# Kernel optimization log

Hardware: AMD Instinct MI355X
Metric: run time of the kernel (lower is better)

## Reference

```python
import jax, jax.numpy as jnp
import numpy as np

HIDDEN = 800
BETA = 0.95
SLOPE = 25.0

@jax.custom_vjp
def surrogate_spike(mem, thr):
    # hard threshold forward, sigmoid-derivative surrogate backward
    return (mem > thr).astype(mem.dtype)

def _spk_fwd(mem, thr):
    return surrogate_spike(mem, thr), (mem, thr)

def _spk_bwd(res, g):
    mem, thr = res
    s = jax.nn.sigmoid(SLOPE * (mem - thr))
    return (g * SLOPE * s * (1.0 - s), jnp.zeros_like(thr))

surrogate_spike.defvjp(_spk_fwd, _spk_bwd)


def setup_inputs() -> dict:
    key = jax.random.key(0)
    ks = jax.random.split(key, 6)
    T, B = 50, 512
    x = jax.random.normal(ks[0], (T, B, 784), dtype=jnp.float32)
    # Kaiming-ish init scaled by 1/sqrt(fan_in)
    W1 = jax.random.normal(ks[1], (HIDDEN, 784), dtype=jnp.float32) / np.sqrt(784.0)
    W2 = jax.random.normal(ks[2], (HIDDEN, HIDDEN), dtype=jnp.float32) / np.sqrt(float(HIDDEN))
    W3 = jax.random.normal(ks[3], (10, HIDDEN), dtype=jnp.float32) / np.sqrt(float(HIDDEN))
    b1 = jnp.zeros((HIDDEN,), jnp.float32)
    b2 = jnp.zeros((HIDDEN,), jnp.float32)
    b3 = jnp.zeros((10,), jnp.float32)
    budget1 = jax.random.uniform(ks[4], (HIDDEN,), dtype=jnp.float32)
    budget2 = jax.random.uniform(ks[5], (HIDDEN,), dtype=jnp.float32)
    return {"x": x, "W1": W1, "b1": b1, "W2": W2, "b2": b2,
            "W3": W3, "b3": b3, "budget1": budget1, "budget2": budget2}


def reference(x, W1, b1, W2, b2, W3, b3, budget1, budget2):
    # thresholds: 1 / clamp(budget / max_budget, 0.01, 1.0); max_budget = 1.0 here
    thr1 = 1.0 / jnp.clip(budget1, 0.01, 1.0)
    thr2 = 1.0 / jnp.clip(budget2, 0.01, 1.0)
    thr3 = jnp.asarray(1.0, x.dtype)
    B = x.shape[1]

    def step(carry, xt):
        m1, m2, m3 = carry
        m1 = BETA * m1 + xt @ W1.T + b1            # [B, HIDDEN]
        s1 = surrogate_spike(m1, thr1)
        m1 = m1 * (1.0 - s1)                        # multiplicative reset
        m2 = BETA * m2 + s1 @ W2.T + b2
        s2 = surrogate_spike(m2, thr2)
        m2 = m2 * (1.0 - s2)
        m3 = BETA * m3 + s2 @ W3.T + b3            # [B, 10]
        s3 = surrogate_spike(m3, thr3)
        m3 = m3 * (1.0 - s3)
        return (m1, m2, m3), (s1, s2, s3)

    init = (jnp.zeros((B, HIDDEN), x.dtype),
            jnp.zeros((B, HIDDEN), x.dtype),
            jnp.zeros((B, 10), x.dtype))
    _, (s1r, s2r, s3r) = jax.lax.scan(step, init, x)
    return (s3r.sum(0), s1r, s2r, s3r)
```

## Files before the change

kernel.cpp:

```cpp
#include <hip/hip_runtime.h>

#define BATCH   512
#define TSTEPS  50
#define NIN     784
#define NHID    800
#define NOUT    10
#define KC      384

typedef float v4f __attribute__((ext_vector_type(4)));

#define ROW_FMA(pl, ph, as)                       \
    pl.x = __fmaf_rn(as, blo.x, pl.x);            \
    pl.y = __fmaf_rn(as, blo.y, pl.y);            \
    pl.z = __fmaf_rn(as, blo.z, pl.z);            \
    pl.w = __fmaf_rn(as, blo.w, pl.w);            \
    ph.x = __fmaf_rn(as, bhi.x, ph.x);            \
    ph.y = __fmaf_rn(as, bhi.y, ph.y);            \
    ph.z = __fmaf_rn(as, bhi.z, ph.z);            \
    ph.w = __fmaf_rn(as, bhi.w, ph.w);

#define STORE_ROW(i, pl, ph)                                        \
    {   float* crow = Cp + (size_t)(m0 + 8*ty + (i)) * N + cb;      \
        if (cb + 4 <= N) *(float4*)crow = pl;                       \
        if (cb + 8 <= N) *(float4*)(crow + 4) = ph; }

__global__ __launch_bounds__(256, 2)
void gemm_panel_f32(const float* __restrict__ A, const float* __restrict__ B,
                    float* __restrict__ Cp, int M, int N, int K,
                    int ks, int ke)
{
    __shared__ float As[8][132];
    __shared__ float Bs[8][188];

    const int tid = threadIdx.x;
    const int tx = tid & 15;
    const int ty = tid >> 4;
    const int m0 = blockIdx.x * 128;
    const int n0 = blockIdx.y * 128;

    const int srow = tid >> 1;
    const int skq  = (tid & 1) * 4;
    const int bphys = 12 * (srow >> 3) + (srow & 7);

    const float* Aptr = A + (size_t)(m0 + srow) * K + skq;
    const float* Bptr = B + (size_t)(n0 + srow) * K + skq;
    const bool bval = (n0 + srow) < N;

    float4 p0l = {0,0,0,0}, p0h = {0,0,0,0}, p1l = {0,0,0,0}, p1h = {0,0,0,0};
    float4 p2l = {0,0,0,0}, p2h = {0,0,0,0}, p3l = {0,0,0,0}, p3h = {0,0,0,0};
    float4 p4l = {0,0,0,0}, p4h = {0,0,0,0}, p5l = {0,0,0,0}, p5h = {0,0,0,0};
    float4 p6l = {0,0,0,0}, p6h = {0,0,0,0}, p7l = {0,0,0,0}, p7h = {0,0,0,0};

    float4 av = *(const float4*)(Aptr + ks);
    float4 bv = bval ? *(const float4*)(Bptr + ks) : make_float4(0.f,0.f,0.f,0.f);

    for (int k0 = ks; k0 < ke; k0 += 8) {
        __syncthreads();
        As[skq+0][srow] = av.x; As[skq+1][srow] = av.y;
        As[skq+2][srow] = av.z; As[skq+3][srow] = av.w;
        Bs[skq+0][bphys] = bv.x; Bs[skq+1][bphys] = bv.y;
        Bs[skq+2][bphys] = bv.z; Bs[skq+3][bphys] = bv.w;
        __syncthreads();

        if (k0 + 8 < ke) {
            av = *(const float4*)(Aptr + k0 + 8);
            bv = bval ? *(const float4*)(Bptr + k0 + 8)
                      : make_float4(0.f,0.f,0.f,0.f);
        }

        #pragma unroll
        for (int kk = 0; kk < 8; ++kk) {
            const float4 alo = *(const float4*)&As[kk][8*ty];
            const float4 ahi = *(const float4*)&As[kk][8*ty + 4];
            const float4 blo = *(const float4*)&Bs[kk][12*tx];
            const float4 bhi = *(const float4*)&Bs[kk][12*tx + 4];
            ROW_FMA(p0l, p0h, alo.x)
            ROW_FMA(p1l, p1h, alo.y)
            ROW_FMA(p2l, p2h, alo.z)
            ROW_FMA(p3l, p3h, alo.w)
            ROW_FMA(p4l, p4h, ahi.x)
            ROW_FMA(p5l, p5h, ahi.y)
            ROW_FMA(p6l, p6h, ahi.z)
            ROW_FMA(p7l, p7h, ahi.w)
        }
    }

    const int cb = n0 + 8 * tx;
    STORE_ROW(0, p0l, p0h)
    STORE_ROW(1, p1l, p1h)
    STORE_ROW(2, p2l, p2h)
    STORE_ROW(3, p3l, p3h)
    STORE_ROW(4, p4l, p4h)
    STORE_ROW(5, p5l, p5h)
    STORE_ROW(6, p6l, p6h)
    STORE_ROW(7, p7l, p7h)
}

__global__ __launch_bounds__(256)
void transpose800(const float* __restrict__ W2, float* __restrict__ W2T)
{
    __shared__ float t[32][33];
    const int tx  = threadIdx.x & 31;
    const int ty8 = threadIdx.x >> 5;
    const int bx = blockIdx.x * 32, by = blockIdx.y * 32;

    #pragma unroll
    for (int r = 0; r < 4; ++r) {
        int a = ty8 + r * 8;
        t[a][tx] = W2[(size_t)(by + a) * 800 + bx + tx];
    }
    __syncthreads();
    #pragma unroll
    for (int r = 0; r < 4; ++r) {
        int a = ty8 + r * 8;
        W2T[(size_t)(bx + a) * 800 + by + tx] = t[tx][a];
    }
}

__global__ __launch_bounds__(256)
void lif_scan_hid1(const float* __restrict__ Z0,
                   const float* __restrict__ Z1,
                   const float* __restrict__ xc,
                   const float* __restrict__ W1,
                   const float* __restrict__ bias,
                   const float* __restrict__ budget,
                   float* __restrict__ mcarry,
                   float* __restrict__ Sout,
                   unsigned long long* __restrict__ bm,
                   int CT, int t0)
{
    __shared__ float W1s[NHID][17];

    const int b = blockIdx.x;
    const int tid = threadIdx.x;
    const int lane = tid & 63;
    const int wave = tid >> 6;

    for (int q = tid; q < NHID * 16; q += 256)
        W1s[q >> 4][q & 15] = W1[(size_t)(q >> 4) * NIN + 768 + (q & 15)];
    __syncthreads();

    float m[4], thr[4], bj[4];
    bool val[4];
    int jjv[4];
    #pragma unroll
    for (int c = 0; c < 4; ++c) {
        const int j = c * 256 + tid;
        val[c] = (j < NHID);
        const int jj = val[c] ? j : 0;
        jjv[c] = jj;
        float bu = budget[jj];
        bu = fminf(fmaxf(bu, 0.01f), 1.0f);
        thr[c] = __fdiv_rn(1.0f, bu);
        bj[c]  = bias[jj];
        m[c]   = mcarry[b * NHID + jj];
    }

    for (int ct = 0; ct < CT; ++ct) {
        const size_t zbase = (size_t)ct * (BATCH * NHID) + (size_t)b * NHID;
        const size_t sbase = (size_t)(t0 + ct) * (BATCH * NHID) + (size_t)b * NHID;
        const float* xr = xc + ((size_t)ct * BATCH + b) * NIN + 768;
        const float4 x0 = *(const float4*)(xr);
        const float4 x1 = *(const float4*)(xr + 4);
        const float4 x2 = *(const float4*)(xr + 8);
        const float4 x3 = *(const float4*)(xr + 12);

        #pragma unroll
        for (int c = 0; c < 4; ++c) {
            const int j = c * 256 + tid;
            bool sp = false;
            if (val[c]) {
                const int jj = jjv[c];
                float z = __fadd_rn(__builtin_nontemporal_load(Z0 + zbase + j),
                                    __builtin_nontemporal_load(Z1 + zbase + j));
                float p3 = 0.0f;
                p3 = __fmaf_rn(x0.x, W1s[jj][0],  p3);
                p3 = __fmaf_rn(x0.y, W1s[jj][1],  p3);
                p3 = __fmaf_rn(x0.z, W1s[jj][2],  p3);
                p3 = __fmaf_rn(x0.w, W1s[jj][3],  p3);
                p3 = __fmaf_rn(x1.x, W1s[jj][4],  p3);
                p3 = __fmaf_rn(x1.y, W1s[jj][5],  p3);
                p3 = __fmaf_rn(x1.z, W1s[jj][6],  p3);
                p3 = __fmaf_rn(x1.w, W1s[jj][7],  p3);
                p3 = __fmaf_rn(x2.x, W1s[jj][8],  p3);
                p3 = __fmaf_rn(x2.y, W1s[jj][9],  p3);
                p3 = __fmaf_rn(x2.z, W1s[jj][10], p3);
                p3 = __fmaf_rn(x2.w, W1s[jj][11], p3);
                p3 = __fmaf_rn(x3.x, W1s[jj][12], p3);
                p3 = __fmaf_rn(x3.y, W1s[jj][13], p3);
                p3 = __fmaf_rn(x3.z, W1s[jj][14], p3);
                p3 = __fmaf_rn(x3.w, W1s[jj][15], p3);
                z = __fadd_rn(z, p3);

                float mm = __fadd_rn(__fadd_rn(__fmul_rn(0.95f, m[c]), z), bj[c]);
                sp = (mm > thr[c]);
                m[c] = sp ? 0.0f : mm;
                __builtin_nontemporal_store(sp ? 1.0f : 0.0f, Sout + sbase + j);
            }
            unsigned long long bits = __ballot(sp);
            if (lane == 0) {
                const int W = c * 4 + wave;
                if (W < 13)
                    bm[((size_t)ct * BATCH + b) * 13 + W] = bits;
            }
        }
    }
    #pragma unroll
    for (int c = 0; c < 4; ++c)
        if (val[c]) mcarry[b * NHID + c * 256 + tid] = m[c];
}

__global__ __launch_bounds__(256)
void lif_scan_hid2(const float* __restrict__ Z0,
                   const float* __restrict__ bias,
                   const float* __restrict__ budget,
                   float* __restrict__ mcarry,
                   float* __restrict__ Sout,
                   int CT, int t0)
{
    const int b = blockIdx.x;
    const int tid = threadIdx.x;

    float m[4], thr[4], bj[4];
    bool val[4];
    #pragma unroll
    for (int c = 0; c < 4; ++c) {
        const int j = c * 256 + tid;
        val[c] = (j < NHID);
        const int jj = val[c] ? j : 0;
        float bu = budget[jj];
        bu = fminf(fmaxf(bu, 0.01f), 1.0f);
        thr[c] = __fdiv_rn(1.0f, bu);
        bj[c]  = bias[jj];
        m[c]   = mcarry[b * NHID + jj];
    }

    for (int ct = 0; ct < CT; ++ct) {
        const size_t zbase = (size_t)ct * (BATCH * NHID) + (size_t)b * NHID;
        const size_t sbase = (size_t)(t0 + ct) * (BATCH * NHID) + (size_t)b * NHID;
        #pragma unroll
        for (int c = 0; c < 4; ++c) {
            const int j = c * 256 + tid;
            if (val[c]) {
                float z = __builtin_nontemporal_load(Z0 + zbase + j);
                float mm = __fadd_rn(__fadd_rn(__fmul_rn(0.95f, m[c]), z), bj[c]);
                bool sp = (mm > thr[c]);
                m[c] = sp ? 0.0f : mm;
                __builtin_nontemporal_store(sp ? 1.0f : 0.0f, Sout + sbase + j);
            }
        }
    }
    #pragma unroll
    for (int c = 0; c < 4; ++c)
        if (val[c]) mcarry[b * NHID + c * 256 + tid] = m[c];
}

__global__ __launch_bounds__(256)
void spmm_spikes(const unsigned long long* __restrict__ bm,
                 const float* __restrict__ W2T,
                 float* __restrict__ Z,
                 int rows)
{
    __shared__ unsigned long long wbuf[13];
    __shared__ unsigned short list[NHID];
    __shared__ int offs[14];

    const int tid = threadIdx.x;
    const int lane = tid & 63;
    const int wave = tid >> 6;
    const int row = blockIdx.x;

    if (tid < 13) wbuf[tid] = bm[(size_t)row * 13 + tid];
    __syncthreads();
    if (tid == 0) {
        int o = 0;
        for (int w = 0; w < 13; ++w) { offs[w] = o; o += __popcll(wbuf[w]); }
        offs[13] = o;
    }
    __syncthreads();
    for (int W = wave; W < 13; W += 4) {
        const unsigned long long bits = wbuf[W];
        const int pre = __popcll(bits & ((1ull << lane) - 1ull));
        if ((bits >> lane) & 1ull)
            list[offs[W] + pre] = (unsigned short)(W * 64 + lane);
    }
    __syncthreads();
    const int nnz = offs[13];

    if (tid < 200) {
        const int n = 4 * tid;
        float p0 = 0.f, p1 = 0.f, p2 = 0.f, p3 = 0.f;
        float a0 = 0.f, a1 = 0.f, a2 = 0.f, a3 = 0.f;
        int p = 0, nextb = KC;
        for (int i = 0; i < nnz; ++i) {
            const int k = list[i];
            while (k >= nextb) {
                if (p == 0) { a0 = p0; a1 = p1; a2 = p2; a3 = p3; }
                else {
                    a0 = __fadd_rn(a0, p0); a1 = __fadd_rn(a1, p1);
                    a2 = __fadd_rn(a2, p2); a3 = __fadd_rn(a3, p3);
                }
                p0 = p1 = p2 = p3 = 0.f; ++p;
                nextb = (nextb == KC) ? 2 * KC : 100000;
            }
            const float4 w = *(const float4*)(W2T + (size_t)k * NHID + n);
            p0 = __fadd_rn(p0, w.x); p1 = __fadd_rn(p1, w.y);
            p2 = __fadd_rn(p2, w.z); p3 = __fadd_rn(p3, w.w);
        }
        while (p < 3) {
            if (p == 0) { a0 = p0; a1 = p1; a2 = p2; a3 = p3; }
            else {
                a0 = __fadd_rn(a0, p0); a1 = __fadd_rn(a1, p1);
                a2 = __fadd_rn(a2, p2); a3 = __fadd_rn(a3, p3);
            }
            p0 = p1 = p2 = p3 = 0.f; ++p;
        }
        *(float4*)(Z + (size_t)row * NHID + n) = make_float4(a0, a1, a2, a3);
    }
}

__global__ __launch_bounds__(256)
void gemm3_f32(const float* __restrict__ S2, const float* __restrict__ W3,
               float* __restrict__ Z3, int rows)
{
    int gid = blockIdx.x * 256 + threadIdx.x;
    if (gid >= rows * NOUT) return;
    const int m = gid / NOUT;
    const int nn = gid % NOUT;
    const float* a = S2 + (size_t)m * NHID;
    const float* wr = W3 + (size_t)nn * NHID;

    float part = 0.0f, acc = 0.0f;
    int p = 0;
    for (int i = 0; i < NHID / 4; ++i) {
        if (i == 96 || i == 192) {
            acc = (p == 0) ? part : __fadd_rn(acc, part);
            part = 0.0f; ++p;
        }
        const v4f a4 = __builtin_nontemporal_load((const v4f*)(a + 4 * i));
        const float4 w4 = *(const float4*)(wr + 4 * i);
        part = __fmaf_rn(a4.x, w4.x, part);
        part = __fmaf_rn(a4.y, w4.y, part);
        part = __fmaf_rn(a4.z, w4.z, part);
        part = __fmaf_rn(a4.w, w4.w, part);
    }
    acc = (p == 0) ? part : __fadd_rn(acc, part);
    Z3[gid] = acc;
}

__global__ __launch_bounds__(256)
void lif_scan_small(const float* __restrict__ Z, const float* __restrict__ bias,
                    float* __restrict__ mcarry, float* __restrict__ Sout,
                    int CT, int t0)
{
    const int idx = blockIdx.x * blockDim.x + threadIdx.x;
    const int total = BATCH * NOUT;
    if (idx >= total) return;
    const int j = idx % NOUT;
    const float thr = 1.0f;
    const float bj = bias[j];

    float m = mcarry[idx];
    for (int ct = 0; ct < CT; ++ct) {
        float z = Z[(size_t)ct * total + idx];
        m = __fadd_rn(__fadd_rn(__fmul_rn(0.95f, m), z), bj);
        float s;
        if (m > thr) { s = 1.0f; m = 0.0f; }
        else         { s = 0.0f; }
        Sout[(size_t)(t0 + ct) * total + idx] = s;
    }
    mcarry[idx] = m;
}

__global__ __launch_bounds__(256)
void sum_t(const float* __restrict__ S3, float* __restrict__ out0)
{
    const int idx = blockIdx.x * blockDim.x + threadIdx.x;
    if (idx >= BATCH * NOUT) return;
    float s = 0.0f;
    for (int t = 0; t < TSTEPS; ++t)
        s += S3[(size_t)t * BATCH * NOUT + idx];
    out0[idx] = s;
}

extern "C" void kernel_launch(void* const* d_in, const int* in_sizes, int n_in,
                              void* d_out, int out_size, void* d_ws, size_t ws_size,
                              hipStream_t stream)
{
    const float* x       = (const float*)d_in[0];
    const float* W1      = (const float*)d_in[1];
    const float* b1      = (const float*)d_in[2];
    const float* W2      = (const float*)d_in[3];
    const float* b2      = (const float*)d_in[4];
    const float* W3      = (const float*)d_in[5];
    const float* b3      = (const float*)d_in[6];
    const float* budget1 = (const float*)d_in[7];
    const float* budget2 = (const float*)d_in[8];

    float* out  = (float*)d_out;
    float* out0 = out;
    float* out1 = out0 + BATCH * NOUT;
    float* out2 = out1 + (size_t)TSTEPS * BATCH * NHID;
    float* out3 = out2 + (size_t)TSTEPS * BATCH * NHID;

    const size_t nBH = (size_t)BATCH * NHID;
    const size_t nBO = (size_t)BATCH * NOUT;
    float* m1c = (float*)d_ws;
    float* m2c = m1c + nBH;
    float* m3c = m2c + nBH;
    float* w2t = m3c + nBO;
    unsigned long long* bmask = (unsigned long long*)(w2t + (size_t)NHID * NHID);
    float* Z = (float*)(bmask + (size_t)TSTEPS * BATCH * 13);

    const size_t fixedF = 2 * nBH + nBO + (size_t)NHID * NHID
                        + (size_t)TSTEPS * BATCH * 13 * 2;
    size_t availF = (ws_size / 4 > fixedF) ? (ws_size / 4 - fixedF) : 0;
    const size_t perT = (size_t)BATCH * (2 * NHID + NOUT);
    int CT = (int)(availF / perT);
    if (CT > TSTEPS) CT = TSTEPS;
    if (CT < 1) CT = 1;

    hipMemsetAsync(d_ws, 0, (2 * nBH + nBO) * sizeof(float), stream);

    {
        dim3 tg(25, 25);
        transpose800<<<tg, 256, 0, stream>>>(W2, w2t);
    }

    for (int t0 = 0; t0 < TSTEPS; t0 += CT) {
        int ct = TSTEPS - t0 < CT ? TSTEPS - t0 : CT;
        int Mrows = ct * BATCH;
        const size_t pstride = (size_t)ct * BATCH * NHID;
        float* Zp0 = Z;
        float* Zp1 = Z + pstride;
        float* Z3  = Z + 2 * pstride;
        const float* xc = x + (size_t)t0 * BATCH * NIN;

        {
            dim3 grid(Mrows / 128, (NHID + 127) / 128);
            gemm_panel_f32<<<grid, 256, 0, stream>>>(xc, W1, Zp0, Mrows, NHID, NIN, 0,   384);
            gemm_panel_f32<<<grid, 256, 0, stream>>>(xc, W1, Zp1, Mrows, NHID, NIN, 384, 768);
        }
        lif_scan_hid1<<<BATCH, 256, 0, stream>>>(
            Zp0, Zp1, xc, W1, b1, budget1, m1c, out1, bmask, ct, t0);

        spmm_spikes<<<Mrows, 256, 0, stream>>>(bmask, w2t, Zp0, Mrows);
        lif_scan_hid2<<<BATCH, 256, 0, stream>>>(
            Zp0, b2, budget2, m2c, out2, ct, t0);

        gemm3_f32<<<(Mrows * NOUT + 255) / 256, 256, 0, stream>>>(
            out2 + (size_t)t0 * BATCH * NHID, W3, Z3, Mrows);
        lif_scan_small<<<(BATCH * NOUT + 255) / 256, 256, 0, stream>>>(
            Z3, b3, m3c, out3, ct, t0);
    }

    sum_t<<<(BATCH * NOUT + 255) / 256, 256, 0, stream>>>(out3, out0);
}
```

Baseline: 840.4 us.

## Batch eight spike rows per SpMM block and use inline-asm FMAs in GEMM

The spike-matrix product now handles eight rows per block. It builds a union list of active columns, each tagged with an 8-bit row mask, so every W2T row load is reused across eight output rows through masked FMAs, with the next load prefetched one step ahead. This cuts the repeated W2T gathers and the per-row list setup. In exchange it does wasted FMAs for columns absent in some rows and uses many more registers. The dense GEMM accumulators are turned into scalar floats updated with inline v_fmac_f32 asm, likely to steer register allocation and scheduling.

```diff
diff --git a/kernel.cpp b/kernel.cpp
--- a/kernel.cpp
+++ b/kernel.cpp
@@ -6,23 +6,23 @@
 #define NHID    800
 #define NOUT    10
 #define KC      384
+#define GRP     8
 
 typedef float v4f __attribute__((ext_vector_type(4)));
 
-#define ROW_FMA(pl, ph, as)                       \
-    pl.x = __fmaf_rn(as, blo.x, pl.x);            \
-    pl.y = __fmaf_rn(as, blo.y, pl.y);            \
-    pl.z = __fmaf_rn(as, blo.z, pl.z);            \
-    pl.w = __fmaf_rn(as, blo.w, pl.w);            \
-    ph.x = __fmaf_rn(as, bhi.x, ph.x);            \
-    ph.y = __fmaf_rn(as, bhi.y, ph.y);            \
-    ph.z = __fmaf_rn(as, bhi.z, ph.z);            \
-    ph.w = __fmaf_rn(as, bhi.w, ph.w);
-
-#define STORE_ROW(i, pl, ph)                                        \
+#define GFMA(c, aa, bb) \
+    asm("v_fmac_f32 %0, %1, %2" : "+v"(c) : "v"(aa), "v"(bb));
+
+#define GROW(r, aa) \
+    GFMA(c##r##0, aa, blo.x) GFMA(c##r##1, aa, blo.y) \
+    GFMA(c##r##2, aa, blo.z) GFMA(c##r##3, aa, blo.w) \
+    GFMA(c##r##4, aa, bhi.x) GFMA(c##r##5, aa, bhi.y) \
+    GFMA(c##r##6, aa, bhi.z) GFMA(c##r##7, aa, bhi.w)
+
+#define GSTORE(i, a0, a1, a2, a3, a4, a5, a6, a7)                   \
     {   float* crow = Cp + (size_t)(m0 + 8*ty + (i)) * N + cb;      \
-        if (cb + 4 <= N) *(float4*)crow = pl;                       \
-        if (cb + 8 <= N) *(float4*)(crow + 4) = ph; }
+        if (cb + 4 <= N) *(float4*)crow = make_float4(a0, a1, a2, a3); \
+        if (cb + 8 <= N) *(float4*)(crow + 4) = make_float4(a4, a5, a6, a7); }
 
 __global__ __launch_bounds__(256, 2)
 void gemm_panel_f32(const float* __restrict__ A, const float* __restrict__ B,
@@ -46,10 +46,14 @@
     const float* Bptr = B + (size_t)(n0 + srow) * K + skq;
     const bool bval = (n0 + srow) < N;
 
-    float4 p0l = {0,0,0,0}, p0h = {0,0,0,0}, p1l = {0,0,0,0}, p1h = {0,0,0,0};
-    float4 p2l = {0,0,0,0}, p2h = {0,0,0,0}, p3l = {0,0,0,0}, p3h = {0,0,0,0};
-    float4 p4l = {0,0,0,0}, p4h = {0,0,0,0}, p5l = {0,0,0,0}, p5h = {0,0,0,0};
-    float4 p6l = {0,0,0,0}, p6h = {0,0,0,0}, p7l = {0,0,0,0}, p7h = {0,0,0,0};
+    float c00=0,c01=0,c02=0,c03=0,c04=0,c05=0,c06=0,c07=0;
+    float c10=0,c11=0,c12=0,c13=0,c14=0,c15=0,c16=0,c17=0;
+    float c20=0,c21=0,c22=0,c23=0,c24=0,c25=0,c26=0,c27=0;
+    float c30=0,c31=0,c32=0,c33=0,c34=0,c35=0,c36=0,c37=0;
+    float c40=0,c41=0,c42=0,c43=0,c44=0,c45=0,c46=0,c47=0;
+    float c50=0,c51=0,c52=0,c53=0,c54=0,c55=0,c56=0,c57=0;
+    float c60=0,c61=0,c62=0,c63=0,c64=0,c65=0,c66=0,c67=0;
+    float c70=0,c71=0,c72=0,c73=0,c74=0,c75=0,c76=0,c77=0;
 
     float4 av = *(const float4*)(Aptr + ks);
     float4 bv = bval ? *(const float4*)(Bptr + ks) : make_float4(0.f,0.f,0.f,0.f);
@@ -74,26 +78,20 @@
             const float4 ahi = *(const float4*)&As[kk][8*ty + 4];
             const float4 blo = *(const float4*)&Bs[kk][12*tx];
             const float4 bhi = *(const float4*)&Bs[kk][12*tx + 4];
-            ROW_FMA(p0l, p0h, alo.x)
-            ROW_FMA(p1l, p1h, alo.y)
-            ROW_FMA(p2l, p2h, alo.z)
-            ROW_FMA(p3l, p3h, alo.w)
-            ROW_FMA(p4l, p4h, ahi.x)
-            ROW_FMA(p5l, p5h, ahi.y)
-            ROW_FMA(p6l, p6h, ahi.z)
-            ROW_FMA(p7l, p7h, ahi.w)
+            GROW(0, alo.x) GROW(1, alo.y) GROW(2, alo.z) GROW(3, alo.w)
+            GROW(4, ahi.x) GROW(5, ahi.y) GROW(6, ahi.z) GROW(7, ahi.w)
         }
     }
 
     const int cb = n0 + 8 * tx;
-    STORE_ROW(0, p0l, p0h)
-    STORE_ROW(1, p1l, p1h)
-    STORE_ROW(2, p2l, p2h)
-    STORE_ROW(3, p3l, p3h)
-    STORE_ROW(4, p4l, p4h)
-    STORE_ROW(5, p5l, p5h)
-    STORE_ROW(6, p6l, p6h)
-    STORE_ROW(7, p7l, p7h)
+    GSTORE(0, c00,c01,c02,c03,c04,c05,c06,c07)
+    GSTORE(1, c10,c11,c12,c13,c14,c15,c16,c17)
+    GSTORE(2, c20,c21,c22,c23,c24,c25,c26,c27)
+    GSTORE(3, c30,c31,c32,c33,c34,c35,c36,c37)
+    GSTORE(4, c40,c41,c42,c43,c44,c45,c46,c47)
+    GSTORE(5, c50,c51,c52,c53,c54,c55,c56,c57)
+    GSTORE(6, c60,c61,c62,c63,c64,c65,c66,c67)
+    GSTORE(7, c70,c71,c72,c73,c74,c75,c76,c77)
 }
 
 __global__ __launch_bounds__(256)
@@ -255,67 +253,121 @@
         if (val[c]) mcarry[b * NHID + c * 256 + tid] = m[c];
 }
 
-__global__ __launch_bounds__(256)
-void spmm_spikes(const unsigned long long* __restrict__ bm,
-                 const float* __restrict__ W2T,
-                 float* __restrict__ Z,
-                 int rows)
-{
-    __shared__ unsigned long long wbuf[13];
-    __shared__ unsigned short list[NHID];
+#define SROW(r) \
+    { const float mf = (float)((m8 >> r) & 1u); \
+      GFMA(p##r##0, mf, wq0.x) GFMA(p##r##1, mf, wq0.y) \
+      GFMA(p##r##2, mf, wq0.z) GFMA(p##r##3, mf, wq0.w) }
+
+#define SFOLD1(r) \
+    { a##r##0 = (p == 0) ? p##r##0 : __fadd_rn(a##r##0, p##r##0); \
+      a##r##1 = (p == 0) ? p##r##1 : __fadd_rn(a##r##1, p##r##1); \
+      a##r##2 = (p == 0) ? p##r##2 : __fadd_rn(a##r##2, p##r##2); \
+      a##r##3 = (p == 0) ? p##r##3 : __fadd_rn(a##r##3, p##r##3); \
+      p##r##0 = p##r##1 = p##r##2 = p##r##3 = 0.f; }
+
+#define SFOLDALL \
+    SFOLD1(0) SFOLD1(1) SFOLD1(2) SFOLD1(3) SFOLD1(4) SFOLD1(5) SFOLD1(6) SFOLD1(7)
+
+__global__ __launch_bounds__(256)
+void spmm_spikes8(const unsigned long long* __restrict__ bm,
+                  const float* __restrict__ W2T,
+                  float* __restrict__ Z,
+                  int rows)
+{
+    __shared__ unsigned long long wbuf[GRP][13];
+    __shared__ unsigned long long uni[13];
     __shared__ int offs[14];
+    __shared__ unsigned int list[NHID];
 
     const int tid = threadIdx.x;
     const int lane = tid & 63;
     const int wave = tid >> 6;
-    const int row = blockIdx.x;
-
-    if (tid < 13) wbuf[tid] = bm[(size_t)row * 13 + tid];
+    const int row0 = blockIdx.x * GRP;
+
+    if (tid < GRP * 13) {
+        const int r = tid / 13, w = tid % 13;
+        wbuf[r][w] = bm[(size_t)(row0 + r) * 13 + w];
+    }
+    __syncthreads();
+    if (tid < 13) {
+        unsigned long long u = 0ull;
+        #pragma unroll
+        for (int r = 0; r < GRP; ++r) u |= wbuf[r][tid];
+        uni[tid] = u;
+    }
     __syncthreads();
     if (tid == 0) {
         int o = 0;
-        for (int w = 0; w < 13; ++w) { offs[w] = o; o += __popcll(wbuf[w]); }
+        for (int w = 0; w < 13; ++w) { offs[w] = o; o += __popcll(uni[w]); }
         offs[13] = o;
     }
     __syncthreads();
-    for (int W = wave; W < 13; W += 4) {
-        const unsigned long long bits = wbuf[W];
-        const int pre = __popcll(bits & ((1ull << lane) - 1ull));
-        if ((bits >> lane) & 1ull)
-            list[offs[W] + pre] = (unsigned short)(W * 64 + lane);
+    for (int w = wave; w < 13; w += 4) {
+        const unsigned long long ub = uni[w];
+        if ((ub >> lane) & 1ull) {
+            const int pre = __popcll(ub & ((1ull << lane) - 1ull));
+            unsigned m8 = 0;
+            #pragma unroll
+            for (int r = 0; r < GRP; ++r)
+                m8 |= (unsigned)((wbuf[r][w] >> lane) & 1ull) << r;
+            list[offs[w] + pre] = ((unsigned)(w * 64 + lane) << 8) | m8;
+        }
     }
     __syncthreads();
-    const int nnz = offs[13];
-
-    if (tid < 200) {
-        const int n = 4 * tid;
-        float p0 = 0.f, p1 = 0.f, p2 = 0.f, p3 = 0.f;
-        float a0 = 0.f, a1 = 0.f, a2 = 0.f, a3 = 0.f;
-        int p = 0, nextb = KC;
-        for (int i = 0; i < nnz; ++i) {
-            const int k = list[i];
+    const int cnt = offs[13];
+
+    const bool act = (tid < 200);
+    const int n = 4 * (act ? tid : 0);
+
+    float p00=0,p01=0,p02=0,p03=0, p10=0,p11=0,p12=0,p13=0;
+    float p20=0,p21=0,p22=0,p23=0, p30=0,p31=0,p32=0,p33=0;
+    float p40=0,p41=0,p42=0,p43=0, p50=0,p51=0,p52=0,p53=0;
+    float p60=0,p61=0,p62=0,p63=0, p70=0,p71=0,p72=0,p73=0;
+    float a00=0,a01=0,a02=0,a03=0, a10=0,a11=0,a12=0,a13=0;
+    float a20=0,a21=0,a22=0,a23=0, a30=0,a31=0,a32=0,a33=0;
+    float a40=0,a41=0,a42=0,a43=0, a50=0,a51=0,a52=0,a53=0;
+    float a60=0,a61=0,a62=0,a63=0, a70=0,a71=0,a72=0,a73=0;
+
+    int p = 0, nextb = KC;
+
+    if (cnt > 0) {
+        unsigned e0 = list[0];
+        float4 wq1 = *(const float4*)(W2T + (size_t)(e0 >> 8) * NHID + n);
+        for (int i = 1; i <= cnt; ++i) {
+            const float4 wq0 = wq1;
+            const unsigned ecur = e0;
+            if (i < cnt) {
+                e0 = list[i];
+                wq1 = *(const float4*)(W2T + (size_t)(e0 >> 8) * NHID + n);
+            }
+            const int k = (int)(ecur >> 8);
             while (k >= nextb) {
-                if (p == 0) { a0 = p0; a1 = p1; a2 = p2; a3 = p3; }
-                else {
-                    a0 = __fadd_rn(a0, p0); a1 = __fadd_rn(a1, p1);
-                    a2 = __fadd_rn(a2, p2); a3 = __fadd_rn(a3, p3);
-                }
-                p0 = p1 = p2 = p3 = 0.f; ++p;
-                nextb = (nextb == KC) ? 2 * KC : 100000;
+                SFOLDALL
+                ++p;
+                nextb = (nextb == KC) ? 2 * KC : 0x7FFFFFFF;
             }
-            const float4 w = *(const float4*)(W2T + (size_t)k * NHID + n);
-            p0 = __fadd_rn(p0, w.x); p1 = __fadd_rn(p1, w.y);
-            p2 = __fadd_rn(p2, w.z); p3 = __fadd_rn(p3, w.w);
-        }
-        while (p < 3) {
-            if (p == 0) { a0 = p0; a1 = p1; a2 = p2; a3 = p3; }
-            else {
-                a0 = __fadd_rn(a0, p0); a1 = __fadd_rn(a1, p1);
-                a2 = __fadd_rn(a2, p2); a3 = __fadd_rn(a3, p3);
-            }
-            p0 = p1 = p2 = p3 = 0.f; ++p;
-        }
-        *(float4*)(Z + (size_t)row * NHID + n) = make_float4(a0, a1, a2, a3);
+            const unsigned m8 = ecur & 255u;
+            SROW(0) SROW(1) SROW(2) SROW(3)
+            SROW(4) SROW(5) SROW(6) SROW(7)
+        }
+    }
+    while (p < 3) {
+        SFOLDALL
+        ++p;
+    }
+
+    if (act) {
+        #pragma unroll 1
+        for (int dummy = 0; dummy < 1; ++dummy) {
+            *(float4*)(Z + (size_t)(row0+0)*NHID + n) = make_float4(a00,a01,a02,a03);
+            *(float4*)(Z + (size_t)(row0+1)*NHID + n) = make_float4(a10,a11,a12,a13);
+            *(float4*)(Z + (size_t)(row0+2)*NHID + n) = make_float4(a20,a21,a22,a23);
+            *(float4*)(Z + (size_t)(row0+3)*NHID + n) = make_float4(a30,a31,a32,a33);
+            *(float4*)(Z + (size_t)(row0+4)*NHID + n) = make_float4(a40,a41,a42,a43);
+            *(float4*)(Z + (size_t)(row0+5)*NHID + n) = make_float4(a50,a51,a52,a53);
+            *(float4*)(Z + (size_t)(row0+6)*NHID + n) = make_float4(a60,a61,a62,a63);
+            *(float4*)(Z + (size_t)(row0+7)*NHID + n) = make_float4(a70,a71,a72,a73);
+        }
     }
 }
 
@@ -444,7 +496,7 @@
         lif_scan_hid1<<<BATCH, 256, 0, stream>>>(
             Zp0, Zp1, xc, W1, b1, budget1, m1c, out1, bmask, ct, t0);
 
-        spmm_spikes<<<Mrows, 256, 0, stream>>>(bmask, w2t, Zp0, Mrows);
+        spmm_spikes8<<<Mrows / GRP, 256, 0, stream>>>(bmask, w2t, Zp0, Mrows);
         lif_scan_hid2<<<BATCH, 256, 0, stream>>>(
             Zp0, b2, budget2, m2c, out2, ct, t0);
 
```

Result: slower. 917.1 us (+9.1%).
